# Kernel tuning notes

Hardware: AMD Instinct MI355X
Metric: run time of the kernel (lower is better)

Reference implementation:

```python
import jax, jax.numpy as jnp
import numpy as np

B, S, H, E, V = 4, 256, 1024, 1024, 50257
PAD = 0
DOM = 0.9   # skipLayersDominance
EPS = 1e-5  # LayerNorm eps (torch default)


def setup_inputs() -> dict:
    key = jax.random.key(0)
    ks = jax.random.split(key, 6)
    emb = jax.random.normal(ks[0], (V, E), jnp.float32) * 0.02
    emb = emb.at[PAD].set(0.0)  # padding_idx row zeroed like nn.Embedding
    labels = jax.random.randint(ks[1], (B, S), 0, V)
    W_in = jax.random.normal(ks[2], (E, H), jnp.float32) * (1.0 / np.sqrt(E))
    b_in = jnp.zeros((H,), jnp.float32)
    # Conv1d(2H, H, kernel_size=1, groups=H) weight -> [H, 2] (per-head pair mix)
    W_sani = jax.random.normal(ks[3], (H, 2), jnp.float32) * (1.0 / np.sqrt(2.0))
    b_sani = jnp.zeros((H,), jnp.float32)
    ln_w = jnp.ones((H,), jnp.float32)
    ln_b = jnp.zeros((H,), jnp.float32)
    W_out = jax.random.normal(ks[4], (H, E), jnp.float32) * (1.0 / np.sqrt(H))
    b_out = jnp.zeros((E,), jnp.float32)
    return dict(labels=labels, emb=emb, W_in=W_in, b_in=b_in, W_sani=W_sani,
                b_sani=b_sani, ln_w=ln_w, ln_b=ln_b, W_out=W_out, b_out=b_out)


def _layernorm(x, w, b):
    mu = x.mean(-1, keepdims=True)
    var = x.var(-1, keepdims=True)
    return (x - mu) * jax.lax.rsqrt(var + EPS) * w + b


def _forward(labels, emb, W_in, b_in, W_sani, b_sani, ln_w, ln_b, W_out, b_out):
    x = emb[labels]                                # [B,S,E] inputsEmbeddings
    h = jax.nn.relu(x @ W_in + b_in)               # [B,S,H] inputState
    pos = jnp.arange(S)

    def step(hidden, L):
        # positions <= L are replaced by blank (zeros) per the torch cat logic
        mask = (pos > L)[None, :, None]
        shifted = jnp.concatenate([jnp.zeros_like(hidden[:, :1]), hidden[:, :-1]], axis=1)
        prev = jnp.where(mask, shifted, 0.0)       # hidden[t-1] for t>L else 0
        curr = jnp.where(mask, hidden, 0.0)        # hidden[t]   for t>L else 0
        # torch stack(dim=1)+reshape(B, 2H, 1) == concat(prev, curr) on features;
        # grouped conv (groups=H, 2 ch/group, k=1): out[g] = W[g,0]*cat[2g] + W[g,1]*cat[2g+1] + b[g]
        pair = jnp.concatenate([prev, curr], axis=-1).reshape(B, S, H, 2)
        out = jax.nn.relu(jnp.einsum('bshc,hc->bsh', pair, W_sani) + b_sani)
        out = out * (1.0 - DOM) + hidden           # skipLayers: + sequentialInputState
        out = _layernorm(out, ln_w, ln_b)           # skipLayersNorm
        return out, None

    h, _ = jax.lax.scan(jax.checkpoint(step), h, jnp.arange(S))
    y = jax.nn.relu(h @ W_out + b_out)             # [B,S,E]
    # torch CrossEntropyLoss with float (soft) targets: classes along dim=1 (S)
    logp = jax.nn.log_softmax(y, axis=1)
    loss = -(x * logp).sum(axis=1).mean()
    return loss


def reference(labels, emb, W_in, b_in, W_sani, b_sani, ln_w, ln_b, W_out, b_out):
    return _forward(labels, emb, W_in, b_in, W_sani, b_sani, ln_w, ln_b, W_out, b_out)
```

## Files before the change

kernel.cpp:

```cpp
#include <hip/hip_runtime.h>
#include <cstdint>

#define H_DIM 1024
#define S_LEN 256
#define NBLK_SCAN 128
#define GDEPTH 16
#define DOMC ((float)(1.0 - 0.9))
#define EPS_LN 1e-5f

typedef float v2f __attribute__((ext_vector_type(2)));

template <int CTRL, int RMASK, bool BC>
__device__ __forceinline__ float dpp_term(float x) {
    return __int_as_float(__builtin_amdgcn_update_dpp(
        0, __float_as_int(x), CTRL, RMASK, 0xf, BC));
}
__device__ __forceinline__ float wave_reduce_sum(float x) {
    x += dpp_term<0x111, 0xf, true>(x);
    x += dpp_term<0x112, 0xf, true>(x);
    x += dpp_term<0x114, 0xf, true>(x);
    x += dpp_term<0x118, 0xf, true>(x);
    x += dpp_term<0x142, 0xa, false>(x);
    x += dpp_term<0x143, 0xc, false>(x);
    return __int_as_float(__builtin_amdgcn_readlane(__float_as_int(x), 63));
}

__device__ __forceinline__ int llc_load_int(const int* p) {
    int v;
    asm volatile("global_load_dword %0, %1, off sc0 sc1\n\ts_waitcnt vmcnt(0)"
                 : "=v"(v) : "v"(p) : "memory");
    return v;
}
__device__ __forceinline__ void llc_store_int(int* p, int v) {
    asm volatile("global_store_dword %0, %1, off sc0 sc1" :: "v"(p), "v"(v)
                 : "memory");
}
__device__ __forceinline__ void llc_store_row_nowait(float* base, const float* h) {
    asm volatile(
        "global_store_dword %16, %0, off sc0 sc1\n\t"
        "global_store_dword %16, %1, off offset:256 sc0 sc1\n\t"
        "global_store_dword %16, %2, off offset:512 sc0 sc1\n\t"
        "global_store_dword %16, %3, off offset:768 sc0 sc1\n\t"
        "global_store_dword %16, %4, off offset:1024 sc0 sc1\n\t"
        "global_store_dword %16, %5, off offset:1280 sc0 sc1\n\t"
        "global_store_dword %16, %6, off offset:1536 sc0 sc1\n\t"
        "global_store_dword %16, %7, off offset:1792 sc0 sc1\n\t"
        "global_store_dword %16, %8, off offset:2048 sc0 sc1\n\t"
        "global_store_dword %16, %9, off offset:2304 sc0 sc1\n\t"
        "global_store_dword %16, %10, off offset:2560 sc0 sc1\n\t"
        "global_store_dword %16, %11, off offset:2816 sc0 sc1\n\t"
        "global_store_dword %16, %12, off offset:3072 sc0 sc1\n\t"
        "global_store_dword %16, %13, off offset:3328 sc0 sc1\n\t"
        "global_store_dword %16, %14, off offset:3584 sc0 sc1\n\t"
        "global_store_dword %16, %15, off offset:3840 sc0 sc1"
        :: "v"(h[0]), "v"(h[1]), "v"(h[2]), "v"(h[3]),
           "v"(h[4]), "v"(h[5]), "v"(h[6]), "v"(h[7]),
           "v"(h[8]), "v"(h[9]), "v"(h[10]), "v"(h[11]),
           "v"(h[12]), "v"(h[13]), "v"(h[14]), "v"(h[15]), "v"(base)
        : "memory");
}
__device__ __forceinline__ void llc_publish_lag1(float* dbase, int* flagp,
                                                 int flagval, const float* h) {
    asm volatile(
        "global_store_dword %16, %0, off sc0 sc1\n\t"
        "global_store_dword %16, %1, off offset:256 sc0 sc1\n\t"
        "global_store_dword %16, %2, off offset:512 sc0 sc1\n\t"
        "global_store_dword %16, %3, off offset:768 sc0 sc1\n\t"
        "global_store_dword %16, %4, off offset:1024 sc0 sc1\n\t"
        "global_store_dword %16, %5, off offset:1280 sc0 sc1\n\t"
        "global_store_dword %16, %6, off offset:1536 sc0 sc1\n\t"
        "global_store_dword %16, %7, off offset:1792 sc0 sc1\n\t"
        "global_store_dword %16, %8, off offset:2048 sc0 sc1\n\t"
        "global_store_dword %16, %9, off offset:2304 sc0 sc1\n\t"
        "global_store_dword %16, %10, off offset:2560 sc0 sc1\n\t"
        "global_store_dword %16, %11, off offset:2816 sc0 sc1\n\t"
        "global_store_dword %16, %12, off offset:3072 sc0 sc1\n\t"
        "global_store_dword %16, %13, off offset:3328 sc0 sc1\n\t"
        "global_store_dword %16, %14, off offset:3584 sc0 sc1\n\t"
        "global_store_dword %16, %15, off offset:3840 sc0 sc1\n\t"
        "s_waitcnt vmcnt(16)\n\t"
        "global_store_dword %17, %18, off sc0 sc1"
        :: "v"(h[0]), "v"(h[1]), "v"(h[2]), "v"(h[3]),
           "v"(h[4]), "v"(h[5]), "v"(h[6]), "v"(h[7]),
           "v"(h[8]), "v"(h[9]), "v"(h[10]), "v"(h[11]),
           "v"(h[12]), "v"(h[13]), "v"(h[14]), "v"(h[15]),
           "v"(dbase), "v"(flagp), "v"(flagval)
        : "memory");
}
__device__ __forceinline__ void llc_release(int* flagp, int flagval) {
    asm volatile("s_waitcnt vmcnt(0)\n\t"
                 "global_store_dword %0, %1, off sc0 sc1"
                 :: "v"(flagp), "v"(flagval) : "memory");
}

__device__ __forceinline__ void dma_slot(const float* gslot, float* stg, int l) {
#pragma unroll
    for (int c = 0; c < 4; ++c)
        __builtin_amdgcn_global_load_lds(
            (const __attribute__((address_space(1))) uint32_t*)(gslot + c * 256 + l * 4),
            (__attribute__((address_space(3))) uint32_t*)(stg + c * 256),
            16, 0, 0x11);
}
__device__ __forceinline__ void flag_dma(const int* fp, int* stgf) {
    __builtin_amdgcn_global_load_lds(
        (const __attribute__((address_space(1))) uint32_t*)fp,
        (__attribute__((address_space(3))) uint32_t*)stgf, 4, 0, 0x11);
}

__device__ __forceinline__ void step_barrier() {
    asm volatile("s_waitcnt lgkmcnt(0)\n\ts_barrier" ::: "memory");
}

__device__ __forceinline__ void make_pairs(const float* hv, v2f* c7, int l) {
    const int s0 = (2 * l) & 63, s1 = (2 * l + 1) & 63;
    const bool hi = (l >= 32);
#pragma unroll
    for (int j = 0; j < 8; ++j) {
        float x0 = __shfl(hv[2 * j], s0, 64);
        float x1 = __shfl(hv[2 * j + 1], s0, 64);
        float y0 = __shfl(hv[2 * j], s1, 64);
        float y1 = __shfl(hv[2 * j + 1], s1, 64);
        c7[j].x = hi ? x1 : x0;
        c7[j].y = hi ? y1 : y0;
    }
}

template <bool GATHER>
__global__ __launch_bounds__(256) void gemm_relu_kernel(
    const float* __restrict__ A, const int* __restrict__ labels,
    const float* __restrict__ emb, const float* __restrict__ W,
    const float* __restrict__ bias, float* __restrict__ out,
    int* __restrict__ prodG, int* __restrict__ consG)
{
    __shared__ float As[16][68];
    __shared__ float Bs[16][64];
    __shared__ int   lab[64];

    const int tid = threadIdx.x;
    const int bx = blockIdx.x & 15;
    const int by = blockIdx.x >> 4;
    const int m0 = by * 64, n0 = bx * 64;

    if (GATHER && blockIdx.x == 0) {
        if (tid < NBLK_SCAN) prodG[tid * 32] = -2;
        else                 consG[(tid - NBLK_SCAN) * 32] = -2;
    }
    if (GATHER && tid < 64) lab[tid] = labels[m0 + tid];
    __syncthreads();

    const int tx = tid & 15, ty = tid >> 4;
    const int mload = tid >> 2;
    const int kq    = (tid & 3) * 4;
    const int kb    = tid >> 4;
    const int nb    = (tid & 15) * 4;

    const float* aBase;
    if (GATHER) aBase = emb + (size_t)lab[mload] * 1024 + kq;
    else        aBase = A   + (size_t)(m0 + mload) * 1024 + kq;
    const float* bBase = W + (size_t)kb * 1024 + n0 + nb;

    float4 a_pre = *(const float4*)aBase;
    float4 b_pre = *(const float4*)bBase;

    float acc[4][4] = {};

    for (int k0 = 0; k0 < 1024; k0 += 16) {
        As[kq + 0][mload] = a_pre.x;
        As[kq + 1][mload] = a_pre.y;
        As[kq + 2][mload] = a_pre.z;
        As[kq + 3][mload] = a_pre.w;
        *(float4*)&Bs[kb][nb] = b_pre;
        __syncthreads();

        if (k0 + 16 < 1024) {
            a_pre = *(const float4*)(aBase + k0 + 16);
            b_pre = *(const float4*)(bBase + (size_t)(k0 + 16) * 1024);
        }

#pragma unroll
        for (int kk = 0; kk < 16; ++kk) {
            float a_[4];
#pragma unroll
            for (int i = 0; i < 4; ++i) a_[i] = As[kk][ty * 4 + i];
            float4 bv = *(const float4*)&Bs[kk][tx * 4];
            float b_[4] = {bv.x, bv.y, bv.z, bv.w};
#pragma unroll
            for (int i = 0; i < 4; ++i)
#pragma unroll
                for (int j = 0; j < 4; ++j)
                    acc[i][j] = fmaf(a_[i], b_[j], acc[i][j]);
        }
        __syncthreads();
    }

    float bias4[4];
#pragma unroll
    for (int j = 0; j < 4; ++j) bias4[j] = bias[n0 + tx * 4 + j];
#pragma unroll
    for (int i = 0; i < 4; ++i) {
        float4 o;
        o.x = fmaxf(acc[i][0] + bias4[0], 0.f);
        o.y = fmaxf(acc[i][1] + bias4[1], 0.f);
        o.z = fmaxf(acc[i][2] + bias4[2], 0.f);
        o.w = fmaxf(acc[i][3] + bias4[3], 0.f);
        *(float4*)&out[(size_t)(m0 + ty * 4 + i) * 1024 + n0 + tx * 4] = o;
    }
}

__global__ __launch_bounds__(512, 1) void scan_kernel(
    const float* __restrict__ h0, float* __restrict__ hf,
    const float* __restrict__ Wsani, const float* __restrict__ bsani,
    const float* __restrict__ lnw, const float* __restrict__ lnb,
    float* __restrict__ gbuf, int* __restrict__ prodG, int* __restrict__ consG)
{
    __shared__ float ring[7][2][H_DIM];
    __shared__ float stg[2][H_DIM];
    __shared__ int   stgflag[64];

    const int tid = threadIdx.x, w = tid >> 6, l = tid & 63;
    const int Bb = blockIdx.x;
    const int b = Bb >> 5, p = Bb & 31;
    const int t = 8 * p + w;
    const int row = b * S_LEN + t;
    const bool hasR = (p < 31);
    const int leftB = Bb - 1, rightB = Bb + 1;

    float w0c[16], w1c[16], bsc[16], lwc[16], lbc[16], hv[16];
#pragma unroll
    for (int i = 0; i < 16; ++i) {
        int h = l + 64 * i;
        w0c[i] = Wsani[2 * h]; w1c[i] = Wsani[2 * h + 1];
        bsc[i] = bsani[h]; lwc[i] = lnw[h]; lbc[i] = lnb[h];
        hv[i] = h0[(size_t)row * H_DIM + h];
    }

    if (tid < 64) stgflag[tid] = -2;

    v2f c7[8];
    if (w < 7) {
#pragma unroll
        for (int i = 0; i < 16; ++i) ring[w][1][l + 64 * i] = hv[i];
    } else {
        if (hasR)
            llc_store_row_nowait(
                gbuf + ((size_t)Bb * GDEPTH + (GDEPTH - 1)) * H_DIM + l, hv);
        make_pairs(hv, c7, l);
    }
    __syncthreads();

    const float inv1024 = 1.f / 1024.f;
    int F = -2, pfL = -3, consCache = -2;
    float vv[16];

    for (int L = 0; L < S_LEN; ++L) {
        const bool active = (L < t);
        if (active) {
            v2f pv[8], cv[8];
            if (w == 0) {
                const int* fp = prodG + leftB * 32;
                asm volatile("s_waitcnt vmcnt(0)" ::: "memory");
                {
                    int fa = ((volatile int*)stgflag)[0];
                    if (fa > F) F = fa;
                }
                if (pfL != L - 1) {
                    while (F < L - 1) {
                        F = __builtin_amdgcn_readfirstlane(llc_load_int(fp));
                        if (F < L - 1) __builtin_amdgcn_s_sleep(1);
                    }
                    dma_slot(gbuf + ((size_t)leftB * GDEPTH +
                                     ((L - 1) & (GDEPTH - 1))) * H_DIM,
                             stg[(L - 1) & 1], l);
                    pfL = L - 1;
                    asm volatile("s_waitcnt vmcnt(0)" ::: "memory");
                }
                const float* srcp = stg[(L - 1) & 1];
#pragma unroll
                for (int j = 0; j < 8; ++j)
                    pv[j] = *(const v2f*)&srcp[2 * l + 128 * j];
#pragma unroll
                for (int j = 0; j < 8; ++j)
                    cv[j] = *(const v2f*)&ring[0][(L - 1) & 1][2 * l + 128 * j];
                if (L < t - 1) {
                    if (F >= L) {
                        dma_slot(gbuf + ((size_t)leftB * GDEPTH +
                                         (L & (GDEPTH - 1))) * H_DIM,
                                 stg[L & 1], l);
                        pfL = L;
                    }
                    flag_dma(fp, stgflag);
                }
                llc_store_int(consG + Bb * 32, L);
            } else {
                const float* srcp = &ring[w - 1][(L - 1) & 1][0];
#pragma unroll
                for (int j = 0; j < 8; ++j)
                    pv[j] = *(const v2f*)&srcp[2 * l + 128 * j];
                if (w < 7) {
                    const float* srcc = &ring[w][(L - 1) & 1][0];
#pragma unroll
                    for (int j = 0; j < 8; ++j)
                        cv[j] = *(const v2f*)&srcc[2 * l + 128 * j];
                } else {
#pragma unroll
                    for (int j = 0; j < 8; ++j) cv[j] = c7[j];
                }
            }
#pragma unroll
            for (int i = 0; i < 8; ++i) {
                float s = fmaf(pv[i].x, w0c[i], fmaf(pv[i].y, w1c[i], bsc[i]));
                s = fmaxf(s, 0.f);
                vv[i] = fmaf(DOMC, s, hv[i]);
            }
#pragma unroll
            for (int i = 8; i < 16; ++i) {
                float s = fmaf(cv[i - 8].x, w0c[i],
                               fmaf(cv[i - 8].y, w1c[i], bsc[i]));
                s = fmaxf(s, 0.f);
                vv[i] = fmaf(DOMC, s, hv[i]);
            }
        } else {
#pragma unroll
            for (int i = 0; i < 16; ++i) {
                float s = fmaxf(bsc[i], 0.f);
                vv[i] = fmaf(DOMC, s, hv[i]);
            }
        }
        float sum = 0.f, ss = 0.f;
#pragma unroll
        for (int i = 0; i < 16; ++i) { sum += vv[i]; ss = fmaf(vv[i], vv[i], ss); }
        sum = wave_reduce_sum(sum); ss = wave_reduce_sum(ss);
        const float mu = sum * inv1024;
        const float var = fmaf(-mu, mu, ss * inv1024);
        const float r = 1.f / sqrtf(var + EPS_LN);
#pragma unroll
        for (int i = 0; i < 16; ++i)
            hv[i] = fmaf((vv[i] - mu) * r, lwc[i], lbc[i]);

        if (active) {
            if (w < 7) {
#pragma unroll
                for (int i = 0; i < 16; ++i) ring[w][L & 1][l + 64 * i] = hv[i];
            } else {
                if (hasR) {
                    if (consCache < L - (GDEPTH - 3)) {
                        int c = llc_load_int(consG + rightB * 32);
                        while (c < L - (GDEPTH - 1)) {
                            __builtin_amdgcn_s_sleep(1);
                            c = llc_load_int(consG + rightB * 32);
                        }
                        consCache = __builtin_amdgcn_readfirstlane(c);
                    }
                    llc_publish_lag1(
                        gbuf + ((size_t)Bb * GDEPTH + (L & (GDEPTH - 1))) * H_DIM + l,
                        prodG + Bb * 32, L - 1, hv);
                }
                if (L + 1 < t) make_pairs(hv, c7, l);
            }
        } else if (w == 7 && hasR && L == t) {
            llc_release(prodG + Bb * 32, t - 1);
        }
        step_barrier();
    }
#pragma unroll
    for (int i = 0; i < 16; ++i)
        hf[(size_t)row * H_DIM + l + 64 * i] = hv[i];
}

__global__ __launch_bounds__(256) void lse_kernel(
    const float* __restrict__ y, float* __restrict__ lse)
{
    const int b = blockIdx.x >> 4, et = blockIdx.x & 15;
    const int col = threadIdx.x & 63, rg = threadIdx.x >> 6;
    const int e = et * 64 + col;
    const float* yb = y + (size_t)b * S_LEN * H_DIM + e;
    float m = -INFINITY, s = 0.f;
    for (int r = rg; r < S_LEN; r += 4) {
        float v = yb[(size_t)r * H_DIM];
        float mn = fmaxf(m, v);
        s = fmaf(s, expf(m - mn), expf(v - mn));
        m = mn;
    }
    __shared__ float sm[4][64], sp[4][64];
    sm[rg][col] = m; sp[rg][col] = s;
    __syncthreads();
    if (threadIdx.x < 64) {
        const int c = threadIdx.x;
        float M = fmaxf(fmaxf(sm[0][c], sm[1][c]), fmaxf(sm[2][c], sm[3][c]));
        float S = sp[0][c] * expf(sm[0][c] - M) + sp[1][c] * expf(sm[1][c] - M)
                + sp[2][c] * expf(sm[2][c] - M) + sp[3][c] * expf(sm[3][c] - M);
        lse[b * H_DIM + et * 64 + c] = M + logf(S);
    }
}

__global__ __launch_bounds__(256) void loss_row_kernel(
    const float* __restrict__ y, const int* __restrict__ labels,
    const float* __restrict__ emb, const float* __restrict__ lse,
    float* __restrict__ partials)
{
    const int bs = blockIdx.x;
    const int b = bs >> 8;
    const int lab = labels[bs];
    const float* yr = y + (size_t)bs * H_DIM;
    const float* er = emb + (size_t)lab * H_DIM;
    const float* lr = lse + b * H_DIM;
    float acc = 0.f;
#pragma unroll
    for (int i = 0; i < 4; ++i) {
        int e = threadIdx.x + 256 * i;
        acc = fmaf(er[e], yr[e] - lr[e], acc);
    }
    acc = wave_reduce_sum(acc);
    __shared__ float wsum[4];
    if ((threadIdx.x & 63) == 0) wsum[threadIdx.x >> 6] = acc;
    __syncthreads();
    if (threadIdx.x == 0)
        partials[bs] = (wsum[0] + wsum[1]) + (wsum[2] + wsum[3]);
}

__global__ __launch_bounds__(256) void loss_final_kernel(
    const float* __restrict__ partials, float* __restrict__ out)
{
    const int tid = threadIdx.x;
    float a = 0.f;
#pragma unroll
    for (int j = 0; j < 4; ++j) a += partials[tid + 256 * j];
    a = wave_reduce_sum(a);
    __shared__ float wsum[4];
    if ((tid & 63) == 0) wsum[tid >> 6] = a;
    __syncthreads();
    if (tid == 0)
        out[0] = -((wsum[0] + wsum[1]) + (wsum[2] + wsum[3])) * (1.f / 4096.f);
}

extern "C" void kernel_launch(void* const* d_in, const int* in_sizes, int n_in,
                              void* d_out, int out_size, void* d_ws, size_t ws_size,
                              hipStream_t stream)
{
    const int*   labels = (const int*)  d_in[0];
    const float* emb    = (const float*)d_in[1];
    const float* W_in   = (const float*)d_in[2];
    const float* b_in   = (const float*)d_in[3];
    const float* W_sani = (const float*)d_in[4];
    const float* b_sani = (const float*)d_in[5];
    const float* ln_w   = (const float*)d_in[6];
    const float* ln_b   = (const float*)d_in[7];
    const float* W_out  = (const float*)d_in[8];
    const float* b_out  = (const float*)d_in[9];
    float* out = (float*)d_out;

    float* ws = (float*)d_ws;
    float* h0       = ws;
    float* hf       = ws + (1 << 20);
    float* yb       = ws + 2 * (1 << 20);
    float* gbuf     = ws + 3 * (1 << 20);
    float* lse      = ws + 5 * (1 << 20);
    float* partials = lse + 4096;
    int*   prodG    = (int*)(partials + 1024);
    int*   consG    = prodG + NBLK_SCAN * 32;

    gemm_relu_kernel<true><<<dim3(256), dim3(256), 0, stream>>>(
        nullptr, labels, emb, W_in, b_in, h0, prodG, consG);
    {
        const float* a_h0 = h0; float* a_hf = hf;
        const float* a_ws = W_sani; const float* a_bs = b_sani;
        const float* a_lw = ln_w;   const float* a_lb = ln_b;
        float* a_gb = gbuf; int* a_pf = prodG; int* a_cf = consG;
        void* args[] = { (void*)&a_h0, (void*)&a_hf, (void*)&a_ws, (void*)&a_bs,
                         (void*)&a_lw, (void*)&a_lb, (void*)&a_gb,
                         (void*)&a_pf, (void*)&a_cf };
        hipLaunchCooperativeKernel((const void*)scan_kernel,
                                   dim3(NBLK_SCAN), dim3(512), args, 0, stream);
    }
    gemm_relu_kernel<false><<<dim3(256), dim3(256), 0, stream>>>(
        hf, nullptr, emb, W_out, b_out, yb, nullptr, nullptr);
    lse_kernel<<<dim3(64), dim3(256), 0, stream>>>(yb, lse);
    loss_row_kernel<<<dim3(1024), dim3(256), 0, stream>>>(
        yb, labels, emb, lse, partials);
    loss_final_kernel<<<dim3(1), dim3(256), 0, stream>>>(partials, out);
}
```

Baseline: 777.2 us.

## Replace per-step block barriers with LDS flag handshakes and a dedicated prefetch wave

Drops the per-step s_barrier in the scan kernel. Waves now hand off ring slots through per-wave producer/consumer flags in LDS, with a 4-deep ring and staging buffer. A ninth wave is added that only polls the left neighbour's global flag and DMAs rows into LDS ahead of time, so wave 0 no longer does the cross-block polling and loading inline. This is meant to let waves run ahead of one another and hide inter-block latency, at the cost of spin-waits on LDS flags, more LDS use, and ordering hazards with the async global_load_lds.

```diff
diff --git a/kernel.cpp b/kernel.cpp
--- a/kernel.cpp
+++ b/kernel.cpp
@@ -101,15 +101,6 @@
             (__attribute__((address_space(3))) uint32_t*)(stg + c * 256),
             16, 0, 0x11);
 }
-__device__ __forceinline__ void flag_dma(const int* fp, int* stgf) {
-    __builtin_amdgcn_global_load_lds(
-        (const __attribute__((address_space(1))) uint32_t*)fp,
-        (__attribute__((address_space(3))) uint32_t*)stgf, 4, 0, 0x11);
-}
-
-__device__ __forceinline__ void step_barrier() {
-    asm volatile("s_waitcnt lgkmcnt(0)\n\ts_barrier" ::: "memory");
-}
 
 __device__ __forceinline__ void make_pairs(const float* hv, v2f* c7, int l) {
     const int s0 = (2 * l) & 63, s1 = (2 * l + 1) & 63;
@@ -207,15 +198,17 @@
     }
 }
 
-__global__ __launch_bounds__(512, 1) void scan_kernel(
+__global__ __launch_bounds__(576, 1) void scan_kernel(
     const float* __restrict__ h0, float* __restrict__ hf,
     const float* __restrict__ Wsani, const float* __restrict__ bsani,
     const float* __restrict__ lnw, const float* __restrict__ lnb,
     float* __restrict__ gbuf, int* __restrict__ prodG, int* __restrict__ consG)
 {
-    __shared__ float ring[7][2][H_DIM];
-    __shared__ float stg[2][H_DIM];
-    __shared__ int   stgflag[64];
+    __shared__ float ring[7][4][H_DIM];
+    __shared__ float stg[4][H_DIM];
+    __shared__ int   srdy[4];
+    __shared__ int   consS;
+    __shared__ int   prodL[8], consL[8];
 
     const int tid = threadIdx.x, w = tid >> 6, l = tid & 63;
     const int Bb = blockIdx.x;
@@ -225,22 +218,26 @@
     const bool hasR = (p < 31);
     const int leftB = Bb - 1, rightB = Bb + 1;
 
+    if (tid < 8) { prodL[tid] = -1; consL[tid] = -1; }
+    if (tid < 4) srdy[tid] = -100;
+    if (tid == 8) consS = -2;
+
     float w0c[16], w1c[16], bsc[16], lwc[16], lbc[16], hv[16];
-#pragma unroll
-    for (int i = 0; i < 16; ++i) {
-        int h = l + 64 * i;
-        w0c[i] = Wsani[2 * h]; w1c[i] = Wsani[2 * h + 1];
-        bsc[i] = bsani[h]; lwc[i] = lnw[h]; lbc[i] = lnb[h];
-        hv[i] = h0[(size_t)row * H_DIM + h];
-    }
-
-    if (tid < 64) stgflag[tid] = -2;
+    if (w < 8) {
+#pragma unroll
+        for (int i = 0; i < 16; ++i) {
+            int h = l + 64 * i;
+            w0c[i] = Wsani[2 * h]; w1c[i] = Wsani[2 * h + 1];
+            bsc[i] = bsani[h]; lwc[i] = lnw[h]; lbc[i] = lnb[h];
+            hv[i] = h0[(size_t)row * H_DIM + h];
+        }
+    }
 
     v2f c7[8];
     if (w < 7) {
 #pragma unroll
-        for (int i = 0; i < 16; ++i) ring[w][1][l + 64 * i] = hv[i];
-    } else {
+        for (int i = 0; i < 16; ++i) ring[w][3][l + 64 * i] = hv[i];
+    } else if (w == 7) {
         if (hasR)
             llc_store_row_nowait(
                 gbuf + ((size_t)Bb * GDEPTH + (GDEPTH - 1)) * H_DIM + l, hv);
@@ -248,8 +245,49 @@
     }
     __syncthreads();
 
+    if (w == 8) {
+        if (p != 0) {
+            const int lastBeat = 8 * p - 2;
+            const int* fp = prodG + leftB * 32;
+            int* cp = consG + Bb * 32;
+            int F = -2;
+            while (F < -1) { F = __builtin_amdgcn_readfirstlane(llc_load_int(fp));
+                             if (F < -1) __builtin_amdgcn_s_sleep(2); }
+            dma_slot(gbuf + ((size_t)leftB * GDEPTH + (GDEPTH - 1)) * H_DIM,
+                     stg[3], l);
+            llc_store_int(cp, -1);
+            while (F < 0) { F = __builtin_amdgcn_readfirstlane(llc_load_int(fp));
+                            if (F < 0) __builtin_amdgcn_s_sleep(2); }
+            dma_slot(gbuf + ((size_t)leftB * GDEPTH + 0) * H_DIM, stg[0], l);
+
+            for (int B = -1; B <= lastBeat; ++B) {
+                if (B == lastBeat)
+                    asm volatile("s_waitcnt vmcnt(0)" ::: "memory");
+                else
+                    asm volatile("s_waitcnt vmcnt(5)" ::: "memory");
+                if (l == 0) ((volatile int*)srdy)[B & 3] = B;
+                llc_store_int(cp, B + 1);
+                const int nxt = B + 2;
+                if (nxt <= lastBeat) {
+                    while (F < nxt) {
+                        F = __builtin_amdgcn_readfirstlane(llc_load_int(fp));
+                        if (F < nxt) __builtin_amdgcn_s_sleep(2);
+                    }
+                    int sp2 = 0;
+                    while (*(volatile int*)&consS < nxt - 4)
+                        { if (++sp2 > 64) __builtin_amdgcn_s_sleep(1); }
+                    asm volatile("" ::: "memory");
+                    dma_slot(gbuf + ((size_t)leftB * GDEPTH +
+                                     (nxt & (GDEPTH - 1))) * H_DIM,
+                             stg[nxt & 3], l);
+                }
+            }
+        }
+        return;
+    }
+
     const float inv1024 = 1.f / 1024.f;
-    int F = -2, pfL = -3, consCache = -2;
+    int consCache = -2;
     float vv[16];
 
     for (int L = 0; L < S_LEN; ++L) {
@@ -257,47 +295,30 @@
         if (active) {
             v2f pv[8], cv[8];
             if (w == 0) {
-                const int* fp = prodG + leftB * 32;
-                asm volatile("s_waitcnt vmcnt(0)" ::: "memory");
-                {
-                    int fa = ((volatile int*)stgflag)[0];
-                    if (fa > F) F = fa;
-                }
-                if (pfL != L - 1) {
-                    while (F < L - 1) {
-                        F = __builtin_amdgcn_readfirstlane(llc_load_int(fp));
-                        if (F < L - 1) __builtin_amdgcn_s_sleep(1);
-                    }
-                    dma_slot(gbuf + ((size_t)leftB * GDEPTH +
-                                     ((L - 1) & (GDEPTH - 1))) * H_DIM,
-                             stg[(L - 1) & 1], l);
-                    pfL = L - 1;
-                    asm volatile("s_waitcnt vmcnt(0)" ::: "memory");
-                }
-                const float* srcp = stg[(L - 1) & 1];
+                int spin = 0;
+                while (((volatile int*)srdy)[(L - 1) & 3] < L - 1)
+                    { if (++spin > 64) __builtin_amdgcn_s_sleep(1); }
+                asm volatile("" ::: "memory");
+                const float* srcp = stg[(L - 1) & 3];
 #pragma unroll
                 for (int j = 0; j < 8; ++j)
                     pv[j] = *(const v2f*)&srcp[2 * l + 128 * j];
 #pragma unroll
                 for (int j = 0; j < 8; ++j)
-                    cv[j] = *(const v2f*)&ring[0][(L - 1) & 1][2 * l + 128 * j];
-                if (L < t - 1) {
-                    if (F >= L) {
-                        dma_slot(gbuf + ((size_t)leftB * GDEPTH +
-                                         (L & (GDEPTH - 1))) * H_DIM,
-                                 stg[L & 1], l);
-                        pfL = L;
-                    }
-                    flag_dma(fp, stgflag);
-                }
-                llc_store_int(consG + Bb * 32, L);
+                    cv[j] = *(const v2f*)&ring[0][(L - 1) & 3][2 * l + 128 * j];
+                asm volatile("s_waitcnt lgkmcnt(0)" ::: "memory");
+                if (l == 0) *(volatile int*)&consS = L - 1;
             } else {
-                const float* srcp = &ring[w - 1][(L - 1) & 1][0];
+                int spin = 0;
+                while (((volatile int*)prodL)[w - 1] < L - 1)
+                    { if (++spin > 64) __builtin_amdgcn_s_sleep(1); }
+                asm volatile("" ::: "memory");
+                const float* srcp = &ring[w - 1][(L - 1) & 3][0];
 #pragma unroll
                 for (int j = 0; j < 8; ++j)
                     pv[j] = *(const v2f*)&srcp[2 * l + 128 * j];
                 if (w < 7) {
-                    const float* srcc = &ring[w][(L - 1) & 1][0];
+                    const float* srcc = &ring[w][(L - 1) & 3][0];
 #pragma unroll
                     for (int j = 0; j < 8; ++j)
                         cv[j] = *(const v2f*)&srcc[2 * l + 128 * j];
@@ -305,6 +326,8 @@
 #pragma unroll
                     for (int j = 0; j < 8; ++j) cv[j] = c7[j];
                 }
+                asm volatile("s_waitcnt lgkmcnt(0)" ::: "memory");
+                if (l == 0) ((volatile int*)consL)[w] = L;
             }
 #pragma unroll
             for (int i = 0; i < 8; ++i) {
@@ -339,8 +362,14 @@
 
         if (active) {
             if (w < 7) {
-#pragma unroll
-                for (int i = 0; i < 16; ++i) ring[w][L & 1][l + 64 * i] = hv[i];
+                int spin = 0;
+                while (((volatile int*)consL)[w + 1] < L - 3)
+                    { if (++spin > 64) __builtin_amdgcn_s_sleep(1); }
+                asm volatile("" ::: "memory");
+#pragma unroll
+                for (int i = 0; i < 16; ++i) ring[w][L & 3][l + 64 * i] = hv[i];
+                __threadfence_block();
+                if (l == 0) ((volatile int*)prodL)[w] = L;
             } else {
                 if (hasR) {
                     if (consCache < L - (GDEPTH - 3)) {
@@ -360,7 +389,6 @@
         } else if (w == 7 && hasR && L == t) {
             llc_release(prodG + Bb * 32, t - 1);
         }
-        step_barrier();
     }
 #pragma unroll
     for (int i = 0; i < 16; ++i)
@@ -470,7 +498,7 @@
                          (void*)&a_lw, (void*)&a_lb, (void*)&a_gb,
                          (void*)&a_pf, (void*)&a_cf };
         hipLaunchCooperativeKernel((const void*)scan_kernel,
-                                   dim3(NBLK_SCAN), dim3(512), args, 0, stream);
+                                   dim3(NBLK_SCAN), dim3(576), args, 0, stream);
     }
     gemm_relu_kernel<false><<<dim3(256), dim3(256), 0, stream>>>(
         hf, nullptr, emb, W_out, b_out, yb, nullptr, nullptr);
```

Measured after the change: 1.045 ms. 1.34x slower.
